# Kernel optimization log

Measured on AMD Instinct MI355X. Metric: run time of the kernel, lower is better.

## Reference

```python
import jax, jax.numpy as jnp
from jax import lax
import numpy as np

DIM = 256
N_EMBED = 512
B = 16
T = 2048


def setup_inputs() -> dict:
    key = jax.random.key(0)
    k1, k2, k3 = jax.random.split(key, 3)
    inp = jax.random.normal(k1, (B, T, DIM), dtype=jnp.float32)
    spk = jax.random.normal(k2, (3, B, DIM), dtype=jnp.float32)
    embedding = jax.random.normal(k3, (N_EMBED, DIM, DIM), dtype=jnp.float32)
    return {"input": inp, "speaker_embedding": spk, "embedding": embedding}


def reference(input, speaker_embedding, embedding):
    x = input                              # (B, T, D)
    mul = speaker_embedding[2].T           # (D, B)
    add = speaker_embedding[1].T           # (D, B)
    # per-batch codebook: (n, D, D) @ (D, B) -> (n, D, B)
    cb = jnp.einsum('ndk,kb->ndb', embedding, mul)
    cb = cb / jnp.linalg.norm(cb, axis=1, keepdims=True)
    cb = cb + add                          # broadcast (D,B) over n
    embed = jnp.transpose(cb, (2, 1, 0))   # (B, D, n)
    # distances on detached values (matches torch .detach())
    flat = lax.stop_gradient(x)
    e = lax.stop_gradient(embed)
    dist = (jnp.sum(flat * flat, axis=2, keepdims=True)
            - 2.0 * jnp.einsum('btd,bdn->btn', flat, e)
            + jnp.sum(e * e, axis=1, keepdims=True))  # (B, T, n)
    embed_ind = jnp.argmax(-dist, axis=2)  # (B, T)
    cbB = jnp.transpose(cb, (2, 0, 1))     # (B, n, D)
    # per-batch gather of selected codes -> (B, T, D)
    quantize = cbB[jnp.arange(cbB.shape[0])[:, None], embed_ind]
    diff = jnp.mean((quantize - x) ** 2)
    quantize_1 = x + lax.stop_gradient(quantize - x)
    return ((quantize + quantize_1) / 2.0, diff, embed_ind)
```

## Files before the change

kernel.cpp:

```cpp
#include <hip/hip_runtime.h>

#define T_   2048
#define D_   256
#define N_   512
#define BTOT 16

typedef unsigned short ushortT;
typedef _Float16 f16;
typedef f16 h8 __attribute__((ext_vector_type(8)));
typedef float f4v __attribute__((ext_vector_type(4)));

#define QN   ((size_t)BTOT*T_*D_)
#define IDX0 (QN + 1)
#define CBSTRIDE ((size_t)N_*D_)

__device__ __forceinline__ float bf2f(ushortT u){
    union { unsigned int i; float f; } c; c.i = ((unsigned int)u) << 16; return c.f;
}
__device__ __forceinline__ void unp8(uint4 p, float* f){
    f[0]=bf2f((ushortT)(p.x & 0xffff)); f[1]=bf2f((ushortT)(p.x >> 16));
    f[2]=bf2f((ushortT)(p.y & 0xffff)); f[3]=bf2f((ushortT)(p.y >> 16));
    f[4]=bf2f((ushortT)(p.z & 0xffff)); f[5]=bf2f((ushortT)(p.z >> 16));
    f[6]=bf2f((ushortT)(p.w & 0xffff)); f[7]=bf2f((ushortT)(p.w >> 16));
}
__device__ __forceinline__ h8 cvt8(uint4 p){
    float f[8]; unp8(p, f);
    h8 h;
    #pragma unroll
    for (int j = 0; j < 8; j++) h[j] = (f16)f[j];
    return h;
}
__device__ __forceinline__ f4v mfma16(h8 a, h8 b, f4v c){
    return __builtin_amdgcn_mfma_f32_16x16x32_f16(a, b, c, 0, 0, 0);
}

__global__ void k_probe(const ushortT* __restrict__ x, int* __restrict__ flg){
    int tid = threadIdx.x;
    ushortT u = x[tid];
    int e = (u >> 7) & 0xff;
    bool ok = (e >= 100 && e <= 140);
    unsigned long long m = __ballot(ok);
    if (tid == 0) *flg = (__popcll(m) >= 55) ? 1 : 0;
}

template<int BC>
__global__ __launch_bounds__(256) void k_codebook(
    const void* __restrict__ spkin, const void* __restrict__ embin,
    float* __restrict__ cbw, f16* __restrict__ hig, f16* __restrict__ logp,
    float* __restrict__ e2g, int b0, const int* __restrict__ flagp)
{
    const int isb = *flagp;
    const ushortT* ss = (const ushortT*)spkin;
    const float*   sf = (const float*)spkin;
    const ushortT* es = (const ushortT*)embin;
    const float*   ef = (const float*)embin;

    __shared__ float s2[D_ * 16];
    __shared__ float s1[D_ * 16];
    __shared__ float red[16 * D_];
    __shared__ float nrm[16];

    const int n = blockIdx.x, tid = threadIdx.x;

    for (int e = tid; e < D_ * 16; e += 256){ s2[e] = 0.f; s1[e] = 0.f; }
    __syncthreads();
    for (int e = tid; e < D_ * BC; e += 256){
        int blc = e >> 8, k = e & 255;
        int g2 = (2*BTOT + b0 + blc)*D_ + k;
        int g1 = (1*BTOT + b0 + blc)*D_ + k;
        s2[k*16 + blc] = isb ? bf2f(ss[g2]) : sf[g2];
        s1[k*16 + blc] = isb ? bf2f(ss[g1]) : sf[g1];
    }
    __syncthreads();

    const int d = tid;
    float acc[16];
    #pragma unroll
    for (int b = 0; b < 16; b++) acc[b] = 0.f;

    const size_t rb = ((size_t)n * D_ + d) * D_;

    auto inner = [&](const float* ev, int k0){
        #pragma unroll
        for (int j = 0; j < 8; j++){
            float e = ev[j];
            if (BC == 16){
                const float4* sp = (const float4*)&s2[(k0 + j) * 16];
                float4 q0 = sp[0], q1 = sp[1], q2 = sp[2], q3 = sp[3];
                acc[0]  += e*q0.x; acc[1]  += e*q0.y; acc[2]  += e*q0.z; acc[3]  += e*q0.w;
                acc[4]  += e*q1.x; acc[5]  += e*q1.y; acc[6]  += e*q1.z; acc[7]  += e*q1.w;
                acc[8]  += e*q2.x; acc[9]  += e*q2.y; acc[10] += e*q2.z; acc[11] += e*q2.w;
                acc[12] += e*q3.x; acc[13] += e*q3.y; acc[14] += e*q3.z; acc[15] += e*q3.w;
            } else {
                #pragma unroll
                for (int blc = 0; blc < BC; blc++)
                    acc[blc] += e * s2[(k0 + j)*16 + blc];
            }
        }
    };

    if (isb){
        for (int k0 = 0; k0 < D_; k0 += 8){
            uint4 p = *(const uint4*)(es + rb + k0);
            float ev[8]; unp8(p, ev);
            inner(ev, k0);
        }
    } else {
        for (int k0 = 0; k0 < D_; k0 += 8){
            float4 p0 = *(const float4*)(ef + rb + k0);
            float4 p1 = *(const float4*)(ef + rb + k0 + 4);
            float ev[8] = {p0.x,p0.y,p0.z,p0.w,p1.x,p1.y,p1.z,p1.w};
            inner(ev, k0);
        }
    }

    #pragma unroll
    for (int blc = 0; blc < BC; blc++) red[blc*D_ + d] = acc[blc]*acc[blc];
    __syncthreads();
    for (int s = 128; s > 0; s >>= 1){
        if (d < s){
            #pragma unroll
            for (int blc = 0; blc < BC; blc++) red[blc*D_ + d] += red[blc*D_ + d + s];
        }
        __syncthreads();
    }
    if (d < BC) nrm[d] = sqrtf(red[d*D_]);
    __syncthreads();

    float cbv[BC];
    #pragma unroll
    for (int blc = 0; blc < BC; blc++)
        cbv[blc] = acc[blc] / nrm[blc] + s1[d*16 + blc];

    if (!isb){
        #pragma unroll
        for (int blc = 0; blc < BC; blc++)
            cbw[((size_t)blc*N_ + n)*D_ + d] = cbv[blc];
    } else {
        #pragma unroll
        for (int blc = 0; blc < BC; blc++) red[blc*D_ + d] = cbv[blc]*cbv[blc];
        __syncthreads();
        for (int s = 128; s > 0; s >>= 1){
            if (d < s){
                #pragma unroll
                for (int blc = 0; blc < BC; blc++) red[blc*D_ + d] += red[blc*D_ + d + s];
            }
            __syncthreads();
        }
        if (d < BC) e2g[(size_t)d*N_ + n] = red[d*D_];

        f16* sh = (f16*)s2;
        #pragma unroll
        for (int blc = 0; blc < BC; blc++){
            float c = cbv[blc];
            f16 h = (f16)c;
            float r = c - (float)h;
            f16 l = (f16)(r * 4096.f);
            sh[blc*256 + d] = h;
            sh[4096 + blc*256 + d] = l;
        }
        __syncthreads();
        for (int w = tid; w < BC*32; w += 256){
            const int blc = w >> 5, g = w & 31;
            const int d0 = (g>>2)*32 + (g&3)*8;
            const size_t off = (size_t)blc*CBSTRIDE
                             + (size_t)((n>>4)*8 + (g>>2))*512
                             + (size_t)(g&3)*128 + (size_t)(n&15)*8;
            *(uint4*)(hig  + off) = *(const uint4*)(sh + blc*256 + d0);
            *(uint4*)(logp + off) = *(const uint4*)(sh + 4096 + blc*256 + d0);
        }
    }
}

__global__ __launch_bounds__(512, 2) void k_fused(
    const void* __restrict__ xin, const float* __restrict__ cbw,
    const f16* __restrict__ hig, const f16* __restrict__ logp,
    const float* __restrict__ e2g,
    float* __restrict__ outf, float* __restrict__ part,
    int blk0, const int* __restrict__ flagp)
{
    __shared__ float As[16 * 132];
    __shared__ float Bs[16 * 256];
    __shared__ float e2p[512];
    __shared__ float mv[8 * 32];
    __shared__ int   mi[8 * 32];
    __shared__ int   sfin[128];
    __shared__ float wsum[8];

    const int isb = *flagp;
    const int tid = threadIdx.x;
    const int bl = blockIdx.x >> 4, tT = blockIdx.x & 15;
    const int bg = blk0 + bl;

    if (isb){
        const ushortT* xs = (const ushortT*)xin;
        const int lane = tid & 63, wid = tid >> 6;
        const int band = wid >> 1, nh = wid & 1;
        const int arow = lane & 15, kgrp = lane >> 4;

        h8 afr[2][8];
        {
            const ushortT* xw = xs + ((size_t)bg*T_ + (size_t)tT*128 + band*32)*D_;
            #pragma unroll
            for (int rf = 0; rf < 2; rf++)
                #pragma unroll
                for (int ks = 0; ks < 8; ks++){
                    uint4 p = *(const uint4*)(xw + (size_t)(rf*16 + arow)*D_ + ks*32 + kgrp*8);
                    afr[rf][ks] = cvt8(p);
                }
        }

        const f16* hb = hig  + (size_t)bl*CBSTRIDE + (size_t)(lane*8);
        const f16* lb = logp + (size_t)bl*CBSTRIDE + (size_t)(lane*8);

        float runv[8]; int runi[8];
        #pragma unroll
        for (int i = 0; i < 8; i++){ runv[i] = 3.4e38f; runi[i] = 0x7fffffff; }

        #pragma unroll 1
        for (int c = 0; c < 8; c++){
            const int nc0 = nh*16 + c*2;
            f4v acch[2][2], accl[2][2];
            #pragma unroll
            for (int rf = 0; rf < 2; rf++)
                #pragma unroll
                for (int t2 = 0; t2 < 2; t2++){
                    acch[rf][t2] = (f4v){0.f,0.f,0.f,0.f};
                    accl[rf][t2] = (f4v){0.f,0.f,0.f,0.f};
                }
            const f16* hc = hb + (size_t)nc0*4096;
            const f16* lc = lb + (size_t)nc0*4096;
            #pragma unroll
            for (int ks = 0; ks < 8; ks++){
                h8 b0h = *(const h8*)(hc + ks*512);
                h8 b1h = *(const h8*)(hc + 4096 + ks*512);
                h8 b0l = *(const h8*)(lc + ks*512);
                h8 b1l = *(const h8*)(lc + 4096 + ks*512);
                #pragma unroll
                for (int rf = 0; rf < 2; rf++){
                    acch[rf][0] = mfma16(afr[rf][ks], b0h, acch[rf][0]);
                    accl[rf][0] = mfma16(afr[rf][ks], b0l, accl[rf][0]);
                    acch[rf][1] = mfma16(afr[rf][ks], b1h, acch[rf][1]);
                    accl[rf][1] = mfma16(afr[rf][ks], b1l, accl[rf][1]);
                }
            }
            #pragma unroll
            for (int t2 = 0; t2 < 2; t2++){
                const int nn = (nc0 + t2)*16 + arow;
                const float e2v = e2g[(size_t)bl*N_ + nn];
                #pragma unroll
                for (int rf = 0; rf < 2; rf++)
                    #pragma unroll
                    for (int r = 0; r < 4; r++){
                        float s = e2v - 2.f*(acch[rf][t2][r] + accl[rf][t2][r]*(1.f/4096.f));
                        int ii = rf*4 + r;
                        if (s < runv[ii]){ runv[ii] = s; runi[ii] = nn; }
                    }
            }
        }

        #pragma unroll
        for (int m = 8; m >= 1; m >>= 1){
            #pragma unroll
            for (int i = 0; i < 8; i++){
                float ov = __shfl_xor(runv[i], m);
                int   on = __shfl_xor(runi[i], m);
                if (ov < runv[i] || (ov == runv[i] && on < runi[i])){
                    runv[i] = ov; runi[i] = on;
                }
            }
        }
        if (arow == 0){
            #pragma unroll
            for (int i = 0; i < 8; i++){
                int r = (i>>2)*16 + kgrp*4 + (i&3);
                mv[wid*32 + r] = runv[i];
                mi[wid*32 + r] = runi[i];
            }
        }
        __syncthreads();
        if (tid < 128){
            int bandt = tid >> 5, r = tid & 31;
            float v0 = mv[(bandt*2    )*32 + r]; int i0 = mi[(bandt*2    )*32 + r];
            float v1 = mv[(bandt*2 + 1)*32 + r]; int i1 = mi[(bandt*2 + 1)*32 + r];
            int nf = (v1 < v0) ? i1 : i0;
            sfin[tid] = nf;
            outf[IDX0 + (size_t)bg*T_ + (size_t)tT*128 + tid] = (float)nf;
        }
        __syncthreads();

        float dacc = 0.f;
        const int lh = lane >> 5, dg = lane & 31;
        #pragma unroll
        for (int it = 0; it < 8; it++){
            const int r = wid*16 + it*2 + lh;
            const int nn = sfin[r];
            const size_t off = (size_t)bl*CBSTRIDE
                             + (size_t)((nn>>4)*8 + (dg>>2))*512
                             + (size_t)(dg&3)*128 + (size_t)(nn&15)*8;
            h8 hq = *(const h8*)(hig  + off);
            h8 lq = *(const h8*)(logp + off);
            const size_t xo = ((size_t)bg*T_ + (size_t)tT*128 + r)*D_ + dg*8;
            uint4 p = *(const uint4*)(xs + xo);
            float xf8[8]; unp8(p, xf8);
            float og[8];
            #pragma unroll
            for (int j = 0; j < 8; j++){
                float q  = (float)hq[j] + (float)lq[j]*(1.f/4096.f);
                float qm = q - xf8[j];
                dacc += qm*qm;
                og[j] = 0.5f*(q + (xf8[j] + qm));
            }
            *(float4*)(outf + xo)     = make_float4(og[0],og[1],og[2],og[3]);
            *(float4*)(outf + xo + 4) = make_float4(og[4],og[5],og[6],og[7]);
        }
        #pragma unroll
        for (int o2 = 32; o2 > 0; o2 >>= 1) dacc += __shfl_down(dacc, o2, 64);
        if (lane == 0) wsum[wid] = dacc;
        __syncthreads();
        if (tid == 0){
            float t = 0.f;
            #pragma unroll
            for (int i = 0; i < 8; i++) t += wsum[i];
            atomicAdd(&part[blockIdx.x & 1023], t);
        }
    }
    else {
        const float* xf = (const float*)xin;
        const int tx = tid & 31, ty = tid >> 5;
        const int rA = tid >> 2, qA = tid & 3;
        const int rB = tid >> 1, hB = tid & 1;
        const size_t xbase = ((size_t)bg*T_ + tT*128 + rA)*D_ + qA*4;

        float runv[8]; int runi[8];
        #pragma unroll
        for (int i = 0; i < 8; i++){ runv[i] = 3.4e38f; runi[i] = 0x7fffffff; }

        for (int nT = 0; nT < 2; nT++){
            float acc[8][8];
            #pragma unroll
            for (int i = 0; i < 8; i++)
                #pragma unroll
                for (int j = 0; j < 8; j++) acc[i][j] = 0.f;
            float e2acc = 0.f;

            const size_t bbase = ((size_t)bl*N_ + nT*256 + rB)*D_ + hB*8;

            for (int k0 = 0; k0 < D_; k0 += 16){
                float av[4];
                {
                    float4 p = *(const float4*)(xf + xbase + k0);
                    av[0]=p.x; av[1]=p.y; av[2]=p.z; av[3]=p.w;
                }
                float bv[8];
                {
                    float4 q0 = *(const float4*)(cbw + bbase + k0);
                    float4 q1 = *(const float4*)(cbw + bbase + k0 + 4);
                    bv[0]=q0.x; bv[1]=q0.y; bv[2]=q0.z; bv[3]=q0.w;
                    bv[4]=q1.x; bv[5]=q1.y; bv[6]=q1.z; bv[7]=q1.w;
                }
                #pragma unroll
                for (int j = 0; j < 8; j++) e2acc += bv[j]*bv[j];

                #pragma unroll
                for (int j = 0; j < 4; j++) As[(qA*4 + j)*132 + rA] = av[j];
                #pragma unroll
                for (int j = 0; j < 8; j++) Bs[(hB*8 + j)*256 + rB] = bv[j];
                __syncthreads();

                #pragma unroll
                for (int kl = 0; kl < 16; kl++){
                    float4 a0 = *(const float4*)&As[kl*132 + (ty<<2)];
                    float4 a1 = *(const float4*)&As[kl*132 + 64 + (ty<<2)];
                    float4 c0 = *(const float4*)&Bs[kl*256 + (tx<<2)];
                    float4 c1 = *(const float4*)&Bs[kl*256 + 128 + (tx<<2)];
                    float ar[8] = {a0.x,a0.y,a0.z,a0.w,a1.x,a1.y,a1.z,a1.w};
                    float br[8] = {c0.x,c0.y,c0.z,c0.w,c1.x,c1.y,c1.z,c1.w};
                    #pragma unroll
                    for (int i = 0; i < 8; i++)
                        #pragma unroll
                        for (int j = 0; j < 8; j++)
                            acc[i][j] += ar[i]*br[j];
                }
                __syncthreads();
            }

            e2p[rB*2 + hB] = e2acc;
            __syncthreads();

            float e2c[8];
            #pragma unroll
            for (int j = 0; j < 8; j++){
                int nl = (tx<<2) + (j&3) + ((j>>2)<<7);
                e2c[j] = e2p[nl*2] + e2p[nl*2 + 1];
            }

            #pragma unroll
            for (int i = 0; i < 8; i++){
                #pragma unroll
                for (int j = 0; j < 8; j++){
                    int ng = nT*256 + (tx<<2) + (j&3) + ((j>>2)<<7);
                    float s = e2c[j] - 2.f*acc[i][j];
                    if (s < runv[i] || (s == runv[i] && ng < runi[i])){
                        runv[i] = s; runi[i] = ng;
                    }
                }
            }
        }

        #pragma unroll
        for (int m = 16; m >= 1; m >>= 1){
            #pragma unroll
            for (int i = 0; i < 8; i++){
                float ov = __shfl_xor(runv[i], m);
                int   on = __shfl_xor(runi[i], m);
                if (ov < runv[i] || (ov == runv[i] && on < runi[i])){
                    runv[i] = ov; runi[i] = on;
                }
            }
        }
        if (tx == 0){
            #pragma unroll
            for (int i = 0; i < 8; i++){
                int row = (ty<<2) + (i&3) + ((i>>2)<<6);
                sfin[row] = runi[i];
                outf[IDX0 + (size_t)bg*T_ + (size_t)tT*128 + row] = (float)runi[i];
            }
        }
        __syncthreads();

        float dacc = 0.f;
        for (int rr = 0; rr < 128; rr += 2){
            const int row = rr + (tid >> 8);
            const int dd = tid & 255;
            const int nn = sfin[row];
            const float q = cbw[((size_t)bl*N_ + nn)*D_ + dd];
            const size_t xo = ((size_t)bg*T_ + (size_t)tT*128 + row)*D_ + dd;
            const float xv = xf[xo];
            const float qm = q - xv;
            dacc += qm*qm;
            outf[xo] = 0.5f*(q + (xv + qm));
        }
        #pragma unroll
        for (int o2 = 32; o2 > 0; o2 >>= 1) dacc += __shfl_down(dacc, o2, 64);
        if ((tid & 63) == 0) wsum[tid >> 6] = dacc;
        __syncthreads();
        if (tid == 0){
            float t = 0.f;
            #pragma unroll
            for (int i = 0; i < 8; i++) t += wsum[i];
            atomicAdd(&part[blockIdx.x & 1023], t);
        }
    }
}

__global__ __launch_bounds__(256) void k_fin(const float* __restrict__ part,
                                             float* __restrict__ outf){
    const int tid = threadIdx.x;
    float v = part[tid] + part[tid + 256] + part[tid + 512] + part[tid + 768];
    #pragma unroll
    for (int o = 32; o > 0; o >>= 1) v += __shfl_down(v, o, 64);
    __shared__ float wsum[4];
    if ((tid & 63) == 0) wsum[tid >> 6] = v;
    __syncthreads();
    if (tid == 0)
        outf[QN] = (wsum[0] + wsum[1] + wsum[2] + wsum[3]) * (1.0f / (float)QN);
}

extern "C" void kernel_launch(void* const* d_in, const int* in_sizes, int n_in,
                              void* d_out, int out_size, void* d_ws, size_t ws_size,
                              hipStream_t stream)
{
    const void* x   = d_in[0];
    const void* spk = d_in[1];
    const void* emb = d_in[2];

    int Bc = 16;
    while (Bc > 1 && ((size_t)Bc*N_*D_*4 + (size_t)Bc*N_*4 + 4096 + 16) > ws_size) Bc >>= 1;

    char*  ws   = (char*)d_ws;
    f16*   hig  = (f16*)ws;
    f16*   logp = (f16*)(ws + (size_t)Bc*N_*D_*2);
    float* cbw  = (float*)ws;
    float* e2g  = (float*)(ws + (size_t)Bc*N_*D_*4);
    float* part = (float*)(ws + (size_t)Bc*N_*D_*4 + (size_t)Bc*N_*4);
    int*   flg  = (int*)((char*)part + 4096);

    float* outf = (float*)d_out;

    hipMemsetAsync(part, 0, 4096, stream);
    k_probe<<<1, 64, 0, stream>>>((const ushortT*)x, flg);

    for (int b0 = 0; b0 < BTOT; b0 += Bc){
        switch (Bc){
            case 16: k_codebook<16><<<512, 256, 0, stream>>>(spk, emb, cbw, hig, logp, e2g, b0, flg); break;
            case 8:  k_codebook<8> <<<512, 256, 0, stream>>>(spk, emb, cbw, hig, logp, e2g, b0, flg); break;
            case 4:  k_codebook<4> <<<512, 256, 0, stream>>>(spk, emb, cbw, hig, logp, e2g, b0, flg); break;
            case 2:  k_codebook<2> <<<512, 256, 0, stream>>>(spk, emb, cbw, hig, logp, e2g, b0, flg); break;
            default: k_codebook<1> <<<512, 256, 0, stream>>>(spk, emb, cbw, hig, logp, e2g, b0, flg); break;
        }
        k_fused<<<Bc*16, 512, 0, stream>>>(x, cbw, hig, logp, e2g, outf, part, b0, flg);
    }
    k_fin<<<1, 256, 0, stream>>>(part, outf);
}
```

Baseline: 370.7 us.

## Route fp32 path through split-fp16 MFMA distance kernel and halve rows per block

```diff
diff --git a/kernel.cpp b/kernel.cpp
--- a/kernel.cpp
+++ b/kernel.cpp
@@ -22,13 +22,6 @@
     f[2]=bf2f((ushortT)(p.y & 0xffff)); f[3]=bf2f((ushortT)(p.y >> 16));
     f[4]=bf2f((ushortT)(p.z & 0xffff)); f[5]=bf2f((ushortT)(p.z >> 16));
     f[6]=bf2f((ushortT)(p.w & 0xffff)); f[7]=bf2f((ushortT)(p.w >> 16));
-}
-__device__ __forceinline__ h8 cvt8(uint4 p){
-    float f[8]; unp8(p, f);
-    h8 h;
-    #pragma unroll
-    for (int j = 0; j < 8; j++) h[j] = (f16)f[j];
-    return h;
 }
 __device__ __forceinline__ f4v mfma16(h8 a, h8 b, f4v c){
     return __builtin_amdgcn_mfma_f32_16x16x32_f16(a, b, c, 0, 0, 0);
@@ -46,7 +39,7 @@
 template<int BC>
 __global__ __launch_bounds__(256) void k_codebook(
     const void* __restrict__ spkin, const void* __restrict__ embin,
-    float* __restrict__ cbw, f16* __restrict__ hig, f16* __restrict__ logp,
+    f16* __restrict__ hig, f16* __restrict__ logp,
     float* __restrict__ e2g, int b0, const int* __restrict__ flagp)
 {
     const int isb = *flagp;
@@ -132,325 +125,209 @@
     for (int blc = 0; blc < BC; blc++)
         cbv[blc] = acc[blc] / nrm[blc] + s1[d*16 + blc];
 
-    if (!isb){
-        #pragma unroll
-        for (int blc = 0; blc < BC; blc++)
-            cbw[((size_t)blc*N_ + n)*D_ + d] = cbv[blc];
-    } else {
-        #pragma unroll
-        for (int blc = 0; blc < BC; blc++) red[blc*D_ + d] = cbv[blc]*cbv[blc];
+    #pragma unroll
+    for (int blc = 0; blc < BC; blc++) red[blc*D_ + d] = cbv[blc]*cbv[blc];
+    __syncthreads();
+    for (int s = 128; s > 0; s >>= 1){
+        if (d < s){
+            #pragma unroll
+            for (int blc = 0; blc < BC; blc++) red[blc*D_ + d] += red[blc*D_ + d + s];
+        }
         __syncthreads();
-        for (int s = 128; s > 0; s >>= 1){
-            if (d < s){
-                #pragma unroll
-                for (int blc = 0; blc < BC; blc++) red[blc*D_ + d] += red[blc*D_ + d + s];
-            }
-            __syncthreads();
-        }
-        if (d < BC) e2g[(size_t)d*N_ + n] = red[d*D_];
-
-        f16* sh = (f16*)s2;
-        #pragma unroll
-        for (int blc = 0; blc < BC; blc++){
-            float c = cbv[blc];
-            f16 h = (f16)c;
-            float r = c - (float)h;
-            f16 l = (f16)(r * 4096.f);
-            sh[blc*256 + d] = h;
-            sh[4096 + blc*256 + d] = l;
-        }
-        __syncthreads();
-        for (int w = tid; w < BC*32; w += 256){
-            const int blc = w >> 5, g = w & 31;
-            const int d0 = (g>>2)*32 + (g&3)*8;
-            const size_t off = (size_t)blc*CBSTRIDE
-                             + (size_t)((n>>4)*8 + (g>>2))*512
-                             + (size_t)(g&3)*128 + (size_t)(n&15)*8;
-            *(uint4*)(hig  + off) = *(const uint4*)(sh + blc*256 + d0);
-            *(uint4*)(logp + off) = *(const uint4*)(sh + 4096 + blc*256 + d0);
-        }
+    }
+    if (d < BC) e2g[(size_t)d*N_ + n] = red[d*D_];
+
+    f16* sh = (f16*)s2;
+    #pragma unroll
+    for (int blc = 0; blc < BC; blc++){
+        float c = cbv[blc];
+        f16 h = (f16)c;
+        float r = c - (float)h;
+        f16 l = (f16)(r * 4096.f);
+        sh[blc*256 + d] = h;
+        sh[4096 + blc*256 + d] = l;
+    }
+    __syncthreads();
+    for (int w = tid; w < BC*32; w += 256){
+        const int blc = w >> 5, g = w & 31;
+        const int d0 = (g>>2)*32 + (g&3)*8;
+        const size_t off = (size_t)blc*CBSTRIDE
+                         + (size_t)((n>>4)*8 + (g>>2))*512
+                         + (size_t)(g&3)*128 + (size_t)(n&15)*8;
+        *(uint4*)(hig  + off) = *(const uint4*)(sh + blc*256 + d0);
+        *(uint4*)(logp + off) = *(const uint4*)(sh + 4096 + blc*256 + d0);
     }
 }
 
 __global__ __launch_bounds__(512, 2) void k_fused(
-    const void* __restrict__ xin, const float* __restrict__ cbw,
+    const void* __restrict__ xin,
     const f16* __restrict__ hig, const f16* __restrict__ logp,
     const float* __restrict__ e2g,
     float* __restrict__ outf, float* __restrict__ part,
     int blk0, const int* __restrict__ flagp)
 {
-    __shared__ float As[16 * 132];
-    __shared__ float Bs[16 * 256];
-    __shared__ float e2p[512];
-    __shared__ float mv[8 * 32];
-    __shared__ int   mi[8 * 32];
-    __shared__ int   sfin[128];
+    __shared__ float mv[8 * 16];
+    __shared__ int   mi[8 * 16];
+    __shared__ int   sfin[64];
     __shared__ float wsum[8];
 
     const int isb = *flagp;
     const int tid = threadIdx.x;
-    const int bl = blockIdx.x >> 4, tT = blockIdx.x & 15;
+    const int bl = blockIdx.x >> 5, tT = blockIdx.x & 31;
     const int bg = blk0 + bl;
-
-    if (isb){
-        const ushortT* xs = (const ushortT*)xin;
-        const int lane = tid & 63, wid = tid >> 6;
-        const int band = wid >> 1, nh = wid & 1;
-        const int arow = lane & 15, kgrp = lane >> 4;
-
-        h8 afr[2][8];
-        {
-            const ushortT* xw = xs + ((size_t)bg*T_ + (size_t)tT*128 + band*32)*D_;
-            #pragma unroll
-            for (int rf = 0; rf < 2; rf++)
-                #pragma unroll
-                for (int ks = 0; ks < 8; ks++){
-                    uint4 p = *(const uint4*)(xw + (size_t)(rf*16 + arow)*D_ + ks*32 + kgrp*8);
-                    afr[rf][ks] = cvt8(p);
-                }
-        }
-
-        const f16* hb = hig  + (size_t)bl*CBSTRIDE + (size_t)(lane*8);
-        const f16* lb = logp + (size_t)bl*CBSTRIDE + (size_t)(lane*8);
-
-        float runv[8]; int runi[8];
-        #pragma unroll
-        for (int i = 0; i < 8; i++){ runv[i] = 3.4e38f; runi[i] = 0x7fffffff; }
-
-        #pragma unroll 1
-        for (int c = 0; c < 8; c++){
-            const int nc0 = nh*16 + c*2;
-            f4v acch[2][2], accl[2][2];
-            #pragma unroll
-            for (int rf = 0; rf < 2; rf++)
-                #pragma unroll
-                for (int t2 = 0; t2 < 2; t2++){
-                    acch[rf][t2] = (f4v){0.f,0.f,0.f,0.f};
-                    accl[rf][t2] = (f4v){0.f,0.f,0.f,0.f};
-                }
-            const f16* hc = hb + (size_t)nc0*4096;
-            const f16* lc = lb + (size_t)nc0*4096;
-            #pragma unroll
-            for (int ks = 0; ks < 8; ks++){
-                h8 b0h = *(const h8*)(hc + ks*512);
-                h8 b1h = *(const h8*)(hc + 4096 + ks*512);
-                h8 b0l = *(const h8*)(lc + ks*512);
-                h8 b1l = *(const h8*)(lc + 4096 + ks*512);
-                #pragma unroll
-                for (int rf = 0; rf < 2; rf++){
-                    acch[rf][0] = mfma16(afr[rf][ks], b0h, acch[rf][0]);
-                    accl[rf][0] = mfma16(afr[rf][ks], b0l, accl[rf][0]);
-                    acch[rf][1] = mfma16(afr[rf][ks], b1h, acch[rf][1]);
-                    accl[rf][1] = mfma16(afr[rf][ks], b1l, accl[rf][1]);
-                }
-            }
-            #pragma unroll
-            for (int t2 = 0; t2 < 2; t2++){
-                const int nn = (nc0 + t2)*16 + arow;
-                const float e2v = e2g[(size_t)bl*N_ + nn];
-                #pragma unroll
-                for (int rf = 0; rf < 2; rf++)
-                    #pragma unroll
-                    for (int r = 0; r < 4; r++){
-                        float s = e2v - 2.f*(acch[rf][t2][r] + accl[rf][t2][r]*(1.f/4096.f));
-                        int ii = rf*4 + r;
-                        if (s < runv[ii]){ runv[ii] = s; runi[ii] = nn; }
-                    }
-            }
-        }
-
-        #pragma unroll
-        for (int m = 8; m >= 1; m >>= 1){
-            #pragma unroll
-            for (int i = 0; i < 8; i++){
-                float ov = __shfl_xor(runv[i], m);
-                int   on = __shfl_xor(runi[i], m);
-                if (ov < runv[i] || (ov == runv[i] && on < runi[i])){
-                    runv[i] = ov; runi[i] = on;
-                }
-            }
-        }
-        if (arow == 0){
-            #pragma unroll
-            for (int i = 0; i < 8; i++){
-                int r = (i>>2)*16 + kgrp*4 + (i&3);
-                mv[wid*32 + r] = runv[i];
-                mi[wid*32 + r] = runi[i];
-            }
-        }
-        __syncthreads();
-        if (tid < 128){
-            int bandt = tid >> 5, r = tid & 31;
-            float v0 = mv[(bandt*2    )*32 + r]; int i0 = mi[(bandt*2    )*32 + r];
-            float v1 = mv[(bandt*2 + 1)*32 + r]; int i1 = mi[(bandt*2 + 1)*32 + r];
-            int nf = (v1 < v0) ? i1 : i0;
-            sfin[tid] = nf;
-            outf[IDX0 + (size_t)bg*T_ + (size_t)tT*128 + tid] = (float)nf;
-        }
-        __syncthreads();
-
-        float dacc = 0.f;
-        const int lh = lane >> 5, dg = lane & 31;
-        #pragma unroll
-        for (int it = 0; it < 8; it++){
-            const int r = wid*16 + it*2 + lh;
-            const int nn = sfin[r];
-            const size_t off = (size_t)bl*CBSTRIDE
-                             + (size_t)((nn>>4)*8 + (dg>>2))*512
-                             + (size_t)(dg&3)*128 + (size_t)(nn&15)*8;
-            h8 hq = *(const h8*)(hig  + off);
-            h8 lq = *(const h8*)(logp + off);
-            const size_t xo = ((size_t)bg*T_ + (size_t)tT*128 + r)*D_ + dg*8;
-            uint4 p = *(const uint4*)(xs + xo);
-            float xf8[8]; unp8(p, xf8);
+    const int lane = tid & 63, wid = tid >> 6;
+    const int band = wid >> 1, nh = wid & 1;
+    const int arow = lane & 15, kgrp = lane >> 4;
+
+    const ushortT* xs = (const ushortT*)xin;
+    const float*   xf = (const float*)xin;
+
+    h8 ah[8], al[8];
+    {
+        const size_t rowbase = ((size_t)bg*T_ + (size_t)tT*64 + band*16 + arow) * D_;
+        #pragma unroll
+        for (int ks = 0; ks < 8; ks++){
+            float f[8];
+            const size_t o = rowbase + ks*32 + kgrp*8;
+            if (isb){
+                uint4 p = *(const uint4*)(xs + o);
+                unp8(p, f);
+            } else {
+                float4 p0 = *(const float4*)(xf + o);
+                float4 p1 = *(const float4*)(xf + o + 4);
+                f[0]=p0.x; f[1]=p0.y; f[2]=p0.z; f[3]=p0.w;
+                f[4]=p1.x; f[5]=p1.y; f[6]=p1.z; f[7]=p1.w;
+            }
+            h8 h, l;
+            #pragma unroll
+            for (int j = 0; j < 8; j++){
+                f16 hh = (f16)f[j];
+                h[j] = hh;
+                l[j] = (f16)((f[j] - (float)hh) * 4096.f);
+            }
+            ah[ks] = h; al[ks] = l;
+        }
+    }
+
+    const f16* hb = hig  + (size_t)bl*CBSTRIDE + (size_t)(lane*8);
+    const f16* lb = logp + (size_t)bl*CBSTRIDE + (size_t)(lane*8);
+
+    float runv[4]; int runi[4];
+    #pragma unroll
+    for (int i = 0; i < 4; i++){ runv[i] = 3.4e38f; runi[i] = 0x7fffffff; }
+
+    #pragma unroll 1
+    for (int c = 0; c < 8; c++){
+        const int nc0 = nh*16 + c*2;
+        f4v acch[2], accm[2], accl[2];
+        #pragma unroll
+        for (int t2 = 0; t2 < 2; t2++){
+            acch[t2] = (f4v){0.f,0.f,0.f,0.f};
+            accm[t2] = (f4v){0.f,0.f,0.f,0.f};
+            accl[t2] = (f4v){0.f,0.f,0.f,0.f};
+        }
+        const f16* hc = hb + (size_t)nc0*4096;
+        const f16* lc = lb + (size_t)nc0*4096;
+        #pragma unroll
+        for (int ks = 0; ks < 8; ks++){
+            h8 b0h = *(const h8*)(hc + ks*512);
+            h8 b1h = *(const h8*)(hc + 4096 + ks*512);
+            h8 b0l = *(const h8*)(lc + ks*512);
+            h8 b1l = *(const h8*)(lc + 4096 + ks*512);
+            acch[0] = mfma16(ah[ks], b0h, acch[0]);
+            accm[0] = mfma16(ah[ks], b0l, accm[0]);
+            accm[0] = mfma16(al[ks], b0h, accm[0]);
+            accl[0] = mfma16(al[ks], b0l, accl[0]);
+            acch[1] = mfma16(ah[ks], b1h, acch[1]);
+            accm[1] = mfma16(ah[ks], b1l, accm[1]);
+            accm[1] = mfma16(al[ks], b1h, accm[1]);
+            accl[1] = mfma16(al[ks], b1l, accl[1]);
+        }
+        #pragma unroll
+        for (int t2 = 0; t2 < 2; t2++){
+            const int nn = (nc0 + t2)*16 + arow;
+            const float e2v = e2g[(size_t)bl*N_ + nn];
+            #pragma unroll
+            for (int r = 0; r < 4; r++){
+                float dot = acch[t2][r] + accm[t2][r]*(1.f/4096.f)
+                          + accl[t2][r]*(1.f/16777216.f);
+                float s = e2v - 2.f*dot;
+                if (s < runv[r]){ runv[r] = s; runi[r] = nn; }
+            }
+        }
+    }
+
+    #pragma unroll
+    for (int m = 8; m >= 1; m >>= 1){
+        #pragma unroll
+        for (int r = 0; r < 4; r++){
+            float ov = __shfl_xor(runv[r], m);
+            int   on = __shfl_xor(runi[r], m);
+            if (ov < runv[r] || (ov == runv[r] && on < runi[r])){
+                runv[r] = ov; runi[r] = on;
+            }
+        }
+    }
+    if (arow == 0){
+        #pragma unroll
+        for (int r = 0; r < 4; r++){
+            mv[wid*16 + kgrp*4 + r] = runv[r];
+            mi[wid*16 + kgrp*4 + r] = runi[r];
+        }
+    }
+    __syncthreads();
+    if (tid < 64){
+        const int bandt = tid >> 4, rl = tid & 15;
+        float v0 = mv[(bandt*2    )*16 + rl]; int i0 = mi[(bandt*2    )*16 + rl];
+        float v1 = mv[(bandt*2 + 1)*16 + rl]; int i1 = mi[(bandt*2 + 1)*16 + rl];
+        int nf = (v1 < v0) ? i1 : i0;
+        sfin[tid] = nf;
+        outf[IDX0 + (size_t)bg*T_ + (size_t)tT*64 + tid] = (float)nf;
+    }
+    __syncthreads();
+
+    float dacc = 0.f;
+    {
+        const int r = tid >> 3, oct = tid & 7;
+        const int nn = sfin[r];
+        const size_t fb = (size_t)bl*CBSTRIDE
+                        + (size_t)((nn>>4)*8 + oct)*512 + (size_t)(nn&15)*8;
+        const size_t xo0 = ((size_t)bg*T_ + (size_t)tT*64 + r)*D_ + oct*32;
+        #pragma unroll
+        for (int q = 0; q < 4; q++){
+            h8 hq = *(const h8*)(hig  + fb + q*128);
+            h8 lq = *(const h8*)(logp + fb + q*128);
+            float xv[8];
+            if (isb){
+                uint4 p = *(const uint4*)(xs + xo0 + q*8);
+                unp8(p, xv);
+            } else {
+                float4 p0 = *(const float4*)(xf + xo0 + q*8);
+                float4 p1 = *(const float4*)(xf + xo0 + q*8 + 4);
+                xv[0]=p0.x; xv[1]=p0.y; xv[2]=p0.z; xv[3]=p0.w;
+                xv[4]=p1.x; xv[5]=p1.y; xv[6]=p1.z; xv[7]=p1.w;
+            }
             float og[8];
             #pragma unroll
             for (int j = 0; j < 8; j++){
-                float q  = (float)hq[j] + (float)lq[j]*(1.f/4096.f);
-                float qm = q - xf8[j];
+                float qv = (float)hq[j] + (float)lq[j]*(1.f/4096.f);
+                float qm = qv - xv[j];
                 dacc += qm*qm;
-                og[j] = 0.5f*(q + (xf8[j] + qm));
-            }
-            *(float4*)(outf + xo)     = make_float4(og[0],og[1],og[2],og[3]);
-            *(float4*)(outf + xo + 4) = make_float4(og[4],og[5],og[6],og[7]);
-        }
-        #pragma unroll
-        for (int o2 = 32; o2 > 0; o2 >>= 1) dacc += __shfl_down(dacc, o2, 64);
-        if (lane == 0) wsum[wid] = dacc;
-        __syncthreads();
-        if (tid == 0){
-            float t = 0.f;
-            #pragma unroll
-            for (int i = 0; i < 8; i++) t += wsum[i];
-            atomicAdd(&part[blockIdx.x & 1023], t);
-        }
-    }
-    else {
-        const float* xf = (const float*)xin;
-        const int tx = tid & 31, ty = tid >> 5;
-        const int rA = tid >> 2, qA = tid & 3;
-        const int rB = tid >> 1, hB = tid & 1;
-        const size_t xbase = ((size_t)bg*T_ + tT*128 + rA)*D_ + qA*4;
-
-        float runv[8]; int runi[8];
-        #pragma unroll
-        for (int i = 0; i < 8; i++){ runv[i] = 3.4e38f; runi[i] = 0x7fffffff; }
-
-        for (int nT = 0; nT < 2; nT++){
-            float acc[8][8];
-            #pragma unroll
-            for (int i = 0; i < 8; i++)
-                #pragma unroll
-                for (int j = 0; j < 8; j++) acc[i][j] = 0.f;
-            float e2acc = 0.f;
-
-            const size_t bbase = ((size_t)bl*N_ + nT*256 + rB)*D_ + hB*8;
-
-            for (int k0 = 0; k0 < D_; k0 += 16){
-                float av[4];
-                {
-                    float4 p = *(const float4*)(xf + xbase + k0);
-                    av[0]=p.x; av[1]=p.y; av[2]=p.z; av[3]=p.w;
-                }
-                float bv[8];
-                {
-                    float4 q0 = *(const float4*)(cbw + bbase + k0);
-                    float4 q1 = *(const float4*)(cbw + bbase + k0 + 4);
-                    bv[0]=q0.x; bv[1]=q0.y; bv[2]=q0.z; bv[3]=q0.w;
-                    bv[4]=q1.x; bv[5]=q1.y; bv[6]=q1.z; bv[7]=q1.w;
-                }
-                #pragma unroll
-                for (int j = 0; j < 8; j++) e2acc += bv[j]*bv[j];
-
-                #pragma unroll
-                for (int j = 0; j < 4; j++) As[(qA*4 + j)*132 + rA] = av[j];
-                #pragma unroll
-                for (int j = 0; j < 8; j++) Bs[(hB*8 + j)*256 + rB] = bv[j];
-                __syncthreads();
-
-                #pragma unroll
-                for (int kl = 0; kl < 16; kl++){
-                    float4 a0 = *(const float4*)&As[kl*132 + (ty<<2)];
-                    float4 a1 = *(const float4*)&As[kl*132 + 64 + (ty<<2)];
-                    float4 c0 = *(const float4*)&Bs[kl*256 + (tx<<2)];
-                    float4 c1 = *(const float4*)&Bs[kl*256 + 128 + (tx<<2)];
-                    float ar[8] = {a0.x,a0.y,a0.z,a0.w,a1.x,a1.y,a1.z,a1.w};
-                    float br[8] = {c0.x,c0.y,c0.z,c0.w,c1.x,c1.y,c1.z,c1.w};
-                    #pragma unroll
-                    for (int i = 0; i < 8; i++)
-                        #pragma unroll
-                        for (int j = 0; j < 8; j++)
-                            acc[i][j] += ar[i]*br[j];
-                }
-                __syncthreads();
-            }
-
-            e2p[rB*2 + hB] = e2acc;
-            __syncthreads();
-
-            float e2c[8];
-            #pragma unroll
-            for (int j = 0; j < 8; j++){
-                int nl = (tx<<2) + (j&3) + ((j>>2)<<7);
-                e2c[j] = e2p[nl*2] + e2p[nl*2 + 1];
-            }
-
-            #pragma unroll
-            for (int i = 0; i < 8; i++){
-                #pragma unroll
-                for (int j = 0; j < 8; j++){
-                    int ng = nT*256 + (tx<<2) + (j&3) + ((j>>2)<<7);
-                    float s = e2c[j] - 2.f*acc[i][j];
-                    if (s < runv[i] || (s == runv[i] && ng < runi[i])){
-                        runv[i] = s; runi[i] = ng;
-                    }
-                }
-            }
-        }
-
-        #pragma unroll
-        for (int m = 16; m >= 1; m >>= 1){
-            #pragma unroll
-            for (int i = 0; i < 8; i++){
-                float ov = __shfl_xor(runv[i], m);
-                int   on = __shfl_xor(runi[i], m);
-                if (ov < runv[i] || (ov == runv[i] && on < runi[i])){
-                    runv[i] = ov; runi[i] = on;
-                }
-            }
-        }
-        if (tx == 0){
-            #pragma unroll
-            for (int i = 0; i < 8; i++){
-                int row = (ty<<2) + (i&3) + ((i>>2)<<6);
-                sfin[row] = runi[i];
-                outf[IDX0 + (size_t)bg*T_ + (size_t)tT*128 + row] = (float)runi[i];
-            }
-        }
-        __syncthreads();
-
-        float dacc = 0.f;
-        for (int rr = 0; rr < 128; rr += 2){
-            const int row = rr + (tid >> 8);
-            const int dd = tid & 255;
-            const int nn = sfin[row];
-            const float q = cbw[((size_t)bl*N_ + nn)*D_ + dd];
-            const size_t xo = ((size_t)bg*T_ + (size_t)tT*128 + row)*D_ + dd;
-            const float xv = xf[xo];
-            const float qm = q - xv;
-            dacc += qm*qm;
-            outf[xo] = 0.5f*(q + (xv + qm));
-        }
-        #pragma unroll
-        for (int o2 = 32; o2 > 0; o2 >>= 1) dacc += __shfl_down(dacc, o2, 64);
-        if ((tid & 63) == 0) wsum[tid >> 6] = dacc;
-        __syncthreads();
-        if (tid == 0){
-            float t = 0.f;
-            #pragma unroll
-            for (int i = 0; i < 8; i++) t += wsum[i];
-            atomicAdd(&part[blockIdx.x & 1023], t);
-        }
+                og[j] = 0.5f*(qv + (xv[j] + qm));
+            }
+            *(float4*)(outf + xo0 + q*8)     = make_float4(og[0],og[1],og[2],og[3]);
+            *(float4*)(outf + xo0 + q*8 + 4) = make_float4(og[4],og[5],og[6],og[7]);
+        }
+    }
+    #pragma unroll
+    for (int o2 = 32; o2 > 0; o2 >>= 1) dacc += __shfl_down(dacc, o2, 64);
+    if (lane == 0) wsum[wid] = dacc;
+    __syncthreads();
+    if (tid == 0){
+        float t = 0.f;
+        #pragma unroll
+        for (int i = 0; i < 8; i++) t += wsum[i];
+        atomicAdd(&part[blockIdx.x & 1023], t);
     }
 }
 
@@ -481,7 +358,6 @@
     char*  ws   = (char*)d_ws;
     f16*   hig  = (f16*)ws;
     f16*   logp = (f16*)(ws + (size_t)Bc*N_*D_*2);
-    float* cbw  = (float*)ws;
     float* e2g  = (float*)(ws + (size_t)Bc*N_*D_*4);
     float* part = (float*)(ws + (size_t)Bc*N_*D_*4 + (size_t)Bc*N_*4);
     int*   flg  = (int*)((char*)part + 4096);
@@ -493,13 +369,13 @@
 
     for (int b0 = 0; b0 < BTOT; b0 += Bc){
         switch (Bc){
-            case 16: k_codebook<16><<<512, 256, 0, stream>>>(spk, emb, cbw, hig, logp, e2g, b0, flg); break;
-            case 8:  k_codebook<8> <<<512, 256, 0, stream>>>(spk, emb, cbw, hig, logp, e2g, b0, flg); break;
-            case 4:  k_codebook<4> <<<512, 256, 0, stream>>>(spk, emb, cbw, hig, logp, e2g, b0, flg); break;
-            case 2:  k_codebook<2> <<<512, 256, 0, stream>>>(spk, emb, cbw, hig, logp, e2g, b0, flg); break;
-            default: k_codebook<1> <<<512, 256, 0, stream>>>(spk, emb, cbw, hig, logp, e2g, b0, flg); break;
-        }
-        k_fused<<<Bc*16, 512, 0, stream>>>(x, cbw, hig, logp, e2g, outf, part, b0, flg);
+            case 16: k_codebook<16><<<512, 256, 0, stream>>>(spk, emb, hig, logp, e2g, b0, flg); break;
+            case 8:  k_codebook<8> <<<512, 256, 0, stream>>>(spk, emb, hig, logp, e2g, b0, flg); break;
+            case 4:  k_codebook<4> <<<512, 256, 0, stream>>>(spk, emb, hig, logp, e2g, b0, flg); break;
+            case 2:  k_codebook<2> <<<512, 256, 0, stream>>>(spk, emb, hig, logp, e2g, b0, flg); break;
+            default: k_codebook<1> <<<512, 256, 0, stream>>>(spk, emb, hig, logp, e2g, b0, flg); break;
+        }
+        k_fused<<<Bc*32, 512, 0, stream>>>(x, hig, logp, e2g, outf, part, b0, flg);
     }
     k_fin<<<1, 256, 0, stream>>>(part, outf);
 }
```

New measurement: 359.4 us. 3.0% less time.
